# Optimization experiments

Measured on AMD Instinct MI355X. Metric: run time of the kernel, lower is better.

Reference implementation:

```python
import jax, jax.numpy as jnp
import numpy as np

IN_FEATS = 512
OUT_FEATS = 512
N = 8192
M = 8192


def setup_inputs() -> dict:
    key = jax.random.key(0)
    k1, k2, k3 = jax.random.split(key, 3)
    feat_p = jax.random.normal(k1, (N, IN_FEATS), dtype=jnp.float32)
    feat_s = jax.random.normal(k2, (M, IN_FEATS), dtype=jnp.float32)
    # He (kaiming uniform) init: bound = sqrt(6 / fan_in)
    bound = float(np.sqrt(6.0 / IN_FEATS))
    weight_a = jax.random.uniform(k3, (IN_FEATS, OUT_FEATS), dtype=jnp.float32,
                                  minval=-bound, maxval=bound)
    return {"feat_p": feat_p, "feat_s": feat_s, "weight_a": weight_a}


def reference(feat_p, feat_s, weight_a):
    h_i = feat_p @ weight_a            # [N, out]
    h_j = feat_s @ weight_a            # [M, out]
    a_ij = jax.nn.relu(h_i @ h_j.T)    # [N, M]
    fro = jnp.sqrt(jnp.sum(a_ij * a_ij))
    alpha = a_ij / fro                 # global Frobenius-norm normalization
    c_i = alpha @ feat_s               # [N, in]
    return c_i
```

## Files before the change

kernel.cpp:

```cpp
#include <hip/hip_runtime.h>
#include <hip/hip_bf16.h>

#define NROWS 8192
#define DIM   512

typedef short v8s __attribute__((ext_vector_type(8)));
typedef float v4f __attribute__((ext_vector_type(4)));

#define ASM_VMCNT(n) asm volatile("s_waitcnt vmcnt(" #n ")" ::: "memory")
#define ASM_LGKM0    asm volatile("s_waitcnt lgkmcnt(0)" ::: "memory")
#define ASM_FENCE    asm volatile("" ::: "memory")
#define BAR          __builtin_amdgcn_s_barrier()

__device__ __forceinline__ short f2bf(float f) {
    union { float f; unsigned u; } v; v.f = f;
    unsigned r = (v.u + 0x7fffu + ((v.u >> 16) & 1u)) >> 16;
    return (short)r;
}

__device__ __forceinline__ void stage16(const void* g, void* l) {
    typedef __attribute__((address_space(1))) const unsigned GA;
    typedef __attribute__((address_space(3))) unsigned LA;
    __builtin_amdgcn_global_load_lds((GA*)(const unsigned*)g, (LA*)(unsigned*)l, 16, 0, 0);
}

__global__ __launch_bounds__(256) void transpose_cast_kernel(
        const float* __restrict__ in, short* __restrict__ out, int R, int C) {
    __shared__ float t[64][33];
    const int r0 = blockIdx.x * 64;
    const int c0 = blockIdx.y * 32;
    const int lrow = threadIdx.x >> 5;
    const int lcol = threadIdx.x & 31;
#pragma unroll
    for (int p = 0; p < 8; ++p)
        t[lrow + 8 * p][lcol] = in[(size_t)(r0 + lrow + 8 * p) * C + c0 + lcol];
    __syncthreads();
    const int oc = threadIdx.x >> 3;
    const int rb = threadIdx.x & 7;
    v8s o;
#pragma unroll
    for (int e = 0; e < 8; ++e) o[e] = f2bf(t[rb * 8 + e][oc]);
    *(v8s*)(out + (size_t)(c0 + oc) * R + r0 + rb * 8) = o;
}

__global__ __launch_bounds__(256) void gemm1_kernel(
        const float* __restrict__ Fp, const float* __restrict__ Fs,
        const short* __restrict__ WT,
        short* __restrict__ Hp, short* __restrict__ Hs) {
    const float* F = blockIdx.y ? Fs : Fp;
    short* H = blockIdx.y ? Hs : Hp;
    const int lane = threadIdx.x & 63;
    const int wid  = threadIdx.x >> 6;
    const int lr = lane & 15, lg = lane >> 4;
    const int r0 = blockIdx.x * 64 + wid * 16;

    v8s a[16];
#pragma unroll
    for (int kk = 0; kk < 16; ++kk) {
        const float* ap = F + (size_t)(r0 + lr) * DIM + kk * 32 + lg * 8;
        float4 f0 = *(const float4*)ap;
        float4 f1 = *(const float4*)(ap + 4);
        v8s t;
        t[0] = f2bf(f0.x); t[1] = f2bf(f0.y); t[2] = f2bf(f0.z); t[3] = f2bf(f0.w);
        t[4] = f2bf(f1.x); t[5] = f2bf(f1.y); t[6] = f2bf(f1.z); t[7] = f2bf(f1.w);
        a[kk] = t;
    }

    for (int ctp = 0; ctp < 16; ++ctp) {
        const int cb = ctp * 32;
        v4f acc0 = {}, acc1 = {};
#pragma unroll
        for (int kk = 0; kk < 16; ++kk) {
            v8s b0 = *(const v8s*)(WT + (size_t)(cb + lr) * DIM + kk * 32 + lg * 8);
            v8s b1 = *(const v8s*)(WT + (size_t)(cb + 16 + lr) * DIM + kk * 32 + lg * 8);
            acc0 = __builtin_amdgcn_mfma_f32_16x16x32_bf16(a[kk], b0, acc0, 0, 0, 0);
            acc1 = __builtin_amdgcn_mfma_f32_16x16x32_bf16(a[kk], b1, acc1, 0, 0, 0);
        }
#pragma unroll
        for (int i = 0; i < 4; ++i) {
            H[(size_t)(r0 + lg * 4 + i) * DIM + cb + lr]      = f2bf(acc0[i]);
            H[(size_t)(r0 + lg * 4 + i) * DIM + cb + 16 + lr] = f2bf(acc1[i]);
        }
    }
}

#define JSPLIT 2
#define JT_PER_BLOCK (NROWS / 64 / JSPLIT)

__device__ __forceinline__ void stage_full(const char* __restrict__ HsB,
        char* ringW, int j0, int tid) {
#pragma unroll
    for (int s = 0; s < 8; ++s) {
        const int L = s * 8192 + tid * 16;
        const int row = L >> 10;
        const int c = (L & 1023) ^ ((row & 7) << 4);
        stage16(HsB + ((size_t)(j0 + row) << 10) + c, ringW + L);
    }
}

__device__ __forceinline__ void load_bF(v8s (&bF)[8], const short* __restrict__ FsT,
        int j, int wid, int lr, int lg) {
#pragma unroll
    for (int ct = 0; ct < 4; ++ct)
#pragma unroll
        for (int kc2 = 0; kc2 < 2; ++kc2)
            bF[ct * 2 + kc2] = *(const v8s*)(FsT +
                (size_t)(wid * 64 + ct * 16 + lr) * NROWS + j + kc2 * 32 + lg * 8);
}

__device__ __forceinline__ void phase_b(const short (*SbR)[72], const v8s* bF,
        v4f (&accC)[16], int lr, int lg) {
    __builtin_amdgcn_s_setprio(1);
#pragma unroll
    for (int kc2 = 0; kc2 < 2; ++kc2)
#pragma unroll
        for (int mt = 0; mt < 4; ++mt) {
            v8s aS = *(const v8s*)&SbR[mt * 16 + lr][kc2 * 32 + lg * 8];
#pragma unroll
            for (int ct = 0; ct < 4; ++ct)
                accC[mt * 4 + ct] = __builtin_amdgcn_mfma_f32_16x16x32_bf16(
                    aS, bF[ct * 2 + kc2], accC[mt * 4 + ct], 0, 0, 0);
        }
    __builtin_amdgcn_s_setprio(0);
}

__global__ __launch_bounds__(512, 2) void fused_kernel(
        const short* __restrict__ Hp, const short* __restrict__ Hs,
        const short* __restrict__ FsT, float* __restrict__ Cacc,
        float* __restrict__ ssq) {
    __shared__ __align__(16) short HsL[2][64][512];
    __shared__ __align__(16) short Sb[2][64][72];

    const int tid  = threadIdx.x;
    const int lane = tid & 63;
    const int wid  = tid >> 6;
    const int lr = lane & 15, lg = lane >> 4;
    const int strip = wid >> 1;
    const int half  = wid & 1;

    const int nwg = gridDim.x * gridDim.y;
    const int bid = blockIdx.x + gridDim.x * blockIdx.y;
    const int cpx = nwg >> 3;
    const int swz = (bid & 7) * cpx + (bid >> 3);
    const int bx = swz % gridDim.x;
    const int by = swz / gridDim.x;

    const int m0  = bx * 64;
    const int jt0 = by * JT_PER_BLOCK;

    v8s afrag[16];
#pragma unroll
    for (int kk = 0; kk < 16; ++kk)
        afrag[kk] = *(const v8s*)(Hp +
            (size_t)(m0 + strip * 16 + lr) * DIM + kk * 32 + lg * 8);

    v4f accC[16] = {};
    v8s bF[8];
    float ssq_l = 0.f;

    stage_full((const char*)Hs, (char*)&HsL[0][0][0], jt0 * 64, tid);
    ASM_VMCNT(0);

    const int xo = (lr & 7) << 4;

    for (int t = 0; t < JT_PER_BLOCK; ++t) {
        const int jcur  = (jt0 + t) * 64;
        const int jnext = (t + 1 < JT_PER_BLOCK) ? jcur + 64 : jt0 * 64;
        const char* ringR = (const char*)&HsL[t & 1][0][0];
        char*       ringW = (char*)&HsL[(t + 1) & 1][0][0];

        BAR;
        ASM_FENCE;

        stage_full((const char*)Hs, ringW, jnext, tid);

        v4f s0 = {}, s1 = {};
        {
            const char* rp0 = ringR + (size_t)(half * 32 + lr) * 1024;
            const char* rp1 = rp0 + 16 * 1024;
            __builtin_amdgcn_s_setprio(1);
#pragma unroll
            for (int kk = 0; kk < 16; ++kk) {
                const int off = (kk * 64 + lg * 16) ^ xo;
                v8s hb0 = *(const v8s*)(rp0 + off);
                v8s hb1 = *(const v8s*)(rp1 + off);
                s0 = __builtin_amdgcn_mfma_f32_16x16x32_bf16(afrag[kk], hb0, s0, 0, 0, 0);
                s1 = __builtin_amdgcn_mfma_f32_16x16x32_bf16(afrag[kk], hb1, s1, 0, 0, 0);
            }
            __builtin_amdgcn_s_setprio(0);
        }

        short (*SbW)[72] = Sb[t & 1];
#pragma unroll
        for (int i = 0; i < 4; ++i) {
            float v0 = fmaxf(s0[i], 0.f), v1 = fmaxf(s1[i], 0.f);
            ssq_l += v0 * v0 + v1 * v1;
            const int r = strip * 16 + lg * 4 + i;
            SbW[r][(half * 2 + 0) * 16 + lr] = f2bf(v0);
            SbW[r][(half * 2 + 1) * 16 + lr] = f2bf(v1);
        }

        if (t > 0) {
            ASM_VMCNT(8);
            phase_b(Sb[(t - 1) & 1], bF, accC, lr, lg);
        }
        ASM_LGKM0;

        ASM_FENCE;
        load_bF(bF, FsT, jcur, wid, lr, lg);
        ASM_VMCNT(8);
    }

    BAR;
    ASM_VMCNT(0);
    phase_b(Sb[(JT_PER_BLOCK - 1) & 1], bF, accC, lr, lg);

    float w = ssq_l;
#pragma unroll
    for (int off = 32; off; off >>= 1) w += __shfl_down(w, off);
    if (lane == 0) atomicAdd(ssq, w);

#pragma unroll
    for (int mt = 0; mt < 4; ++mt)
#pragma unroll
        for (int ct = 0; ct < 4; ++ct)
#pragma unroll
            for (int i = 0; i < 4; ++i)
                atomicAdd(&Cacc[(size_t)(m0 + mt * 16 + lg * 4 + i) * DIM +
                                wid * 64 + ct * 16 + lr],
                          accC[mt * 4 + ct][i]);
}

__global__ __launch_bounds__(256) void scale_kernel(float* __restrict__ C,
                                                    const float* __restrict__ ssq) {
    const float rs = 1.0f / sqrtf(*ssq);
    const size_t i = (size_t)blockIdx.x * blockDim.x + threadIdx.x;
    float4* p = (float4*)C;
    float4 v = p[i];
    v.x *= rs; v.y *= rs; v.z *= rs; v.w *= rs;
    p[i] = v;
}

extern "C" void kernel_launch(void* const* d_in, const int* in_sizes, int n_in,
                              void* d_out, int out_size, void* d_ws, size_t ws_size,
                              hipStream_t stream) {
    const float* feat_p   = (const float*)d_in[0];
    const float* feat_s   = (const float*)d_in[1];
    const float* weight_a = (const float*)d_in[2];

    char* ws = (char*)d_ws;
    float* ssqp = (float*)ws;
    short* WT   = (short*)(ws + 512);
    short* Hp   = (short*)(ws + 512 + 524288);
    short* Hs   = (short*)(ws + 512 + 524288 + 8388608);
    short* FsT  = (short*)(ws + 512 + 524288 + 16777216);

    transpose_cast_kernel<<<dim3(DIM / 64, DIM / 32), 256, 0, stream>>>(weight_a, WT, DIM, DIM);
    transpose_cast_kernel<<<dim3(NROWS / 64, DIM / 32), 256, 0, stream>>>(feat_s, FsT, NROWS, DIM);

    gemm1_kernel<<<dim3(NROWS / 64, 2), 256, 0, stream>>>(
        feat_p, feat_s, WT, Hp, Hs);

    hipMemsetAsync(d_out, 0, (size_t)out_size * sizeof(float), stream);
    hipMemsetAsync(ssqp, 0, sizeof(float), stream);

    fused_kernel<<<dim3(NROWS / 64, JSPLIT), 512, 0, stream>>>(Hp, Hs, FsT, (float*)d_out, ssqp);

    scale_kernel<<<(out_size / 4 + 255) / 256, 256, 0, stream>>>((float*)d_out, ssqp);
}
```

Measured before the change: 359.7 us.

## Shrink fused kernel tile to 32x32 with 256-thread blocks and split-K accumulators

Reduces the fused GEMM tile from 64 M-rows by 64 J-columns per step to 32x32, using 4 waves per block instead of 8, which doubles the grid size. The phase-A score computation now splits the K loop into even and odd accumulators and sums them, keeping two independent MFMA chains per wave. Phase B is reorganized so each wave covers 128 output columns with 8 B-fragments. The goal is better load balance and occupancy, at the cost of re-reading Hs and FsT twice as often across blocks, more barriers per unit of work, and twice as many atomic adds.

```diff
diff --git a/kernel.cpp b/kernel.cpp
--- a/kernel.cpp
+++ b/kernel.cpp
@@ -84,14 +84,16 @@
     }
 }
 
+#define MTILE  32
+#define JSTEP  32
 #define JSPLIT 2
-#define JT_PER_BLOCK (NROWS / 64 / JSPLIT)
+#define JT_PER_BLOCK (NROWS / JSTEP / JSPLIT)
 
 __device__ __forceinline__ void stage_full(const char* __restrict__ HsB,
         char* ringW, int j0, int tid) {
 #pragma unroll
     for (int s = 0; s < 8; ++s) {
-        const int L = s * 8192 + tid * 16;
+        const int L = s * 4096 + tid * 16;
         const int row = L >> 10;
         const int c = (L & 1023) ^ ((row & 7) << 4);
         stage16(HsB + ((size_t)(j0 + row) << 10) + c, ringW + L);
@@ -101,35 +103,31 @@
 __device__ __forceinline__ void load_bF(v8s (&bF)[8], const short* __restrict__ FsT,
         int j, int wid, int lr, int lg) {
 #pragma unroll
-    for (int ct = 0; ct < 4; ++ct)
-#pragma unroll
-        for (int kc2 = 0; kc2 < 2; ++kc2)
-            bF[ct * 2 + kc2] = *(const v8s*)(FsT +
-                (size_t)(wid * 64 + ct * 16 + lr) * NROWS + j + kc2 * 32 + lg * 8);
-}
-
-__device__ __forceinline__ void phase_b(const short (*SbR)[72], const v8s* bF,
+    for (int ct = 0; ct < 8; ++ct)
+        bF[ct] = *(const v8s*)(FsT +
+            (size_t)(wid * 128 + ct * 16 + lr) * NROWS + j + lg * 8);
+}
+
+__device__ __forceinline__ void phase_b(const short (*SbR)[40], const v8s* bF,
         v4f (&accC)[16], int lr, int lg) {
     __builtin_amdgcn_s_setprio(1);
 #pragma unroll
-    for (int kc2 = 0; kc2 < 2; ++kc2)
-#pragma unroll
-        for (int mt = 0; mt < 4; ++mt) {
-            v8s aS = *(const v8s*)&SbR[mt * 16 + lr][kc2 * 32 + lg * 8];
-#pragma unroll
-            for (int ct = 0; ct < 4; ++ct)
-                accC[mt * 4 + ct] = __builtin_amdgcn_mfma_f32_16x16x32_bf16(
-                    aS, bF[ct * 2 + kc2], accC[mt * 4 + ct], 0, 0, 0);
-        }
+    for (int mt = 0; mt < 2; ++mt) {
+        v8s aS = *(const v8s*)&SbR[mt * 16 + lr][lg * 8];
+#pragma unroll
+        for (int ct = 0; ct < 8; ++ct)
+            accC[mt * 8 + ct] = __builtin_amdgcn_mfma_f32_16x16x32_bf16(
+                aS, bF[ct], accC[mt * 8 + ct], 0, 0, 0);
+    }
     __builtin_amdgcn_s_setprio(0);
 }
 
-__global__ __launch_bounds__(512, 2) void fused_kernel(
+__global__ __launch_bounds__(256, 2) void fused_kernel(
         const short* __restrict__ Hp, const short* __restrict__ Hs,
         const short* __restrict__ FsT, float* __restrict__ Cacc,
         float* __restrict__ ssq) {
-    __shared__ __align__(16) short HsL[2][64][512];
-    __shared__ __align__(16) short Sb[2][64][72];
+    __shared__ __align__(16) short HsL[2][32][512];
+    __shared__ __align__(16) short Sb[2][32][40];
 
     const int tid  = threadIdx.x;
     const int lane = tid & 63;
@@ -145,7 +143,7 @@
     const int bx = swz % gridDim.x;
     const int by = swz / gridDim.x;
 
-    const int m0  = bx * 64;
+    const int m0  = bx * MTILE;
     const int jt0 = by * JT_PER_BLOCK;
 
     v8s afrag[16];
@@ -158,14 +156,14 @@
     v8s bF[8];
     float ssq_l = 0.f;
 
-    stage_full((const char*)Hs, (char*)&HsL[0][0][0], jt0 * 64, tid);
+    stage_full((const char*)Hs, (char*)&HsL[0][0][0], jt0 * JSTEP, tid);
     ASM_VMCNT(0);
 
     const int xo = (lr & 7) << 4;
 
     for (int t = 0; t < JT_PER_BLOCK; ++t) {
-        const int jcur  = (jt0 + t) * 64;
-        const int jnext = (t + 1 < JT_PER_BLOCK) ? jcur + 64 : jt0 * 64;
+        const int jcur  = (jt0 + t) * JSTEP;
+        const int jnext = (t + 1 < JT_PER_BLOCK) ? jcur + JSTEP : jt0 * JSTEP;
         const char* ringR = (const char*)&HsL[t & 1][0][0];
         char*       ringW = (char*)&HsL[(t + 1) & 1][0][0];
 
@@ -174,30 +172,27 @@
 
         stage_full((const char*)Hs, ringW, jnext, tid);
 
-        v4f s0 = {}, s1 = {};
+        v4f sE = {}, sO = {};
         {
-            const char* rp0 = ringR + (size_t)(half * 32 + lr) * 1024;
-            const char* rp1 = rp0 + 16 * 1024;
+            const char* rp = ringR + (size_t)(half * 16 + lr) * 1024;
             __builtin_amdgcn_s_setprio(1);
 #pragma unroll
-            for (int kk = 0; kk < 16; ++kk) {
-                const int off = (kk * 64 + lg * 16) ^ xo;
-                v8s hb0 = *(const v8s*)(rp0 + off);
-                v8s hb1 = *(const v8s*)(rp1 + off);
-                s0 = __builtin_amdgcn_mfma_f32_16x16x32_bf16(afrag[kk], hb0, s0, 0, 0, 0);
-                s1 = __builtin_amdgcn_mfma_f32_16x16x32_bf16(afrag[kk], hb1, s1, 0, 0, 0);
+            for (int kp = 0; kp < 8; ++kp) {
+                const int k0 = 2 * kp, k1 = 2 * kp + 1;
+                v8s hbE = *(const v8s*)(rp + ((k0 * 64 + lg * 16) ^ xo));
+                v8s hbO = *(const v8s*)(rp + ((k1 * 64 + lg * 16) ^ xo));
+                sE = __builtin_amdgcn_mfma_f32_16x16x32_bf16(afrag[k0], hbE, sE, 0, 0, 0);
+                sO = __builtin_amdgcn_mfma_f32_16x16x32_bf16(afrag[k1], hbO, sO, 0, 0, 0);
             }
             __builtin_amdgcn_s_setprio(0);
         }
 
-        short (*SbW)[72] = Sb[t & 1];
+        short (*SbW)[40] = Sb[t & 1];
 #pragma unroll
         for (int i = 0; i < 4; ++i) {
-            float v0 = fmaxf(s0[i], 0.f), v1 = fmaxf(s1[i], 0.f);
-            ssq_l += v0 * v0 + v1 * v1;
-            const int r = strip * 16 + lg * 4 + i;
-            SbW[r][(half * 2 + 0) * 16 + lr] = f2bf(v0);
-            SbW[r][(half * 2 + 1) * 16 + lr] = f2bf(v1);
+            float v = fmaxf(sE[i] + sO[i], 0.f);
+            ssq_l += v * v;
+            SbW[strip * 16 + lg * 4 + i][half * 16 + lr] = f2bf(v);
         }
 
         if (t > 0) {
@@ -221,14 +216,14 @@
     if (lane == 0) atomicAdd(ssq, w);
 
 #pragma unroll
-    for (int mt = 0; mt < 4; ++mt)
-#pragma unroll
-        for (int ct = 0; ct < 4; ++ct)
+    for (int mt = 0; mt < 2; ++mt)
+#pragma unroll
+        for (int ct = 0; ct < 8; ++ct)
 #pragma unroll
             for (int i = 0; i < 4; ++i)
                 atomicAdd(&Cacc[(size_t)(m0 + mt * 16 + lg * 4 + i) * DIM +
-                                wid * 64 + ct * 16 + lr],
-                          accC[mt * 4 + ct][i]);
+                                wid * 128 + ct * 16 + lr],
+                          accC[mt * 8 + ct][i]);
 }
 
 __global__ __launch_bounds__(256) void scale_kernel(float* __restrict__ C,
@@ -264,7 +259,8 @@
     hipMemsetAsync(d_out, 0, (size_t)out_size * sizeof(float), stream);
     hipMemsetAsync(ssqp, 0, sizeof(float), stream);
 
-    fused_kernel<<<dim3(NROWS / 64, JSPLIT), 512, 0, stream>>>(Hp, Hs, FsT, (float*)d_out, ssqp);
+    fused_kernel<<<dim3(NROWS / MTILE, JSPLIT), 256, 0, stream>>>(
+        Hp, Hs, FsT, (float*)d_out, ssqp);
 
     scale_kernel<<<(out_size / 4 + 255) / 256, 256, 0, stream>>>((float*)d_out, ssqp);
 }
```

Result: slower. 464.0 us (+29.0%).

## Split fused attention into materialized S GEMM plus separate C GEMM

Applied to the files above, without the earlier changes.

Replaces the fused kernel (which computed relu(Hp·Hs^T) and multiplied it by feat_s on the fly) with two plain tiled GEMMs when the workspace is large enough. The first writes relu(S) as a 128 MB bf16 matrix and accumulates the sum of squares; the second multiplies S by FsT into the output, so the separate output memset and atomic accumulation go away. The aim is better MFMA tile efficiency and occupancy than the fused kernel, paid for with a large extra round trip of S through HBM. The fused path stays as a fallback when the workspace is too small.

```diff
diff --git a/kernel.cpp b/kernel.cpp
--- a/kernel.cpp
+++ b/kernel.cpp
@@ -84,6 +84,186 @@
     }
 }
 
+__device__ __forceinline__ void stage_t64(const char* __restrict__ src,
+        size_t stride, char* dst, size_t kbyte, int tid) {
+#pragma unroll
+    for (int s = 0; s < 4; ++s) {
+        const int L = s * 4096 + tid * 16;
+        const int row = L >> 7;
+        const int c = (L & 127) ^ ((row & 7) << 4);
+        stage16(src + (size_t)row * stride + kbyte + c, dst + L);
+    }
+}
+
+__device__ __forceinline__ void stage_t128(const char* __restrict__ src,
+        size_t stride, char* dst, size_t kbyte, int tid) {
+#pragma unroll
+    for (int s = 0; s < 8; ++s) {
+        const int L = s * 4096 + tid * 16;
+        const int row = L >> 8;
+        const int c = (L & 255) ^ ((row & 15) << 4);
+        stage16(src + (size_t)row * stride + kbyte + c, dst + L);
+    }
+}
+
+__global__ __launch_bounds__(256, 2) void gemm_s_kernel(
+        const short* __restrict__ Hp, const short* __restrict__ Hs,
+        short* __restrict__ S, float* __restrict__ ssq) {
+    __shared__ __align__(16) short Ab[2][128][64];
+    __shared__ __align__(16) short Bb[2][128][64];
+
+    const int tid = threadIdx.x;
+    const int lane = tid & 63, wq = tid >> 6;
+    const int lr = lane & 15, lg = lane >> 4;
+    const int wm = wq >> 1, wn = wq & 1;
+
+    const int nwg = gridDim.x * gridDim.y;
+    const int bid = blockIdx.x + gridDim.x * blockIdx.y;
+    const int cpx = nwg >> 3;
+    const int swz = (bid & 7) * cpx + (bid >> 3);
+    const int bx = swz % gridDim.x;
+    const int by = swz / gridDim.x;
+    const size_t m0 = (size_t)bx * 128, j0 = (size_t)by * 128;
+
+    const char* Ag = (const char*)Hp + m0 * 1024;
+    const char* Bg = (const char*)Hs + j0 * 1024;
+
+    v4f acc[16] = {};
+
+    stage_t64(Ag, 1024, (char*)&Ab[0][0][0], 0, tid);
+    stage_t64(Bg, 1024, (char*)&Bb[0][0][0], 0, tid);
+    ASM_VMCNT(0);
+
+    const int xo = (lr & 7) << 4;
+    for (int kt = 0; kt < 8; ++kt) {
+        BAR; ASM_FENCE;
+        const size_t kn = (kt + 1 < 8) ? (size_t)(kt + 1) * 128 : 0;
+        stage_t64(Ag, 1024, (char*)&Ab[(kt + 1) & 1][0][0], kn, tid);
+        stage_t64(Bg, 1024, (char*)&Bb[(kt + 1) & 1][0][0], kn, tid);
+
+        const char* Abase = (const char*)&Ab[kt & 1][0][0];
+        const char* Bbase = (const char*)&Bb[kt & 1][0][0];
+        __builtin_amdgcn_s_setprio(1);
+#pragma unroll
+        for (int kc = 0; kc < 2; ++kc) {
+            const int off = (kc * 64 + lg * 16) ^ xo;
+            v8s af[4], bfr[4];
+#pragma unroll
+            for (int mt = 0; mt < 4; ++mt)
+                af[mt] = *(const v8s*)(Abase + (wm * 64 + mt * 16 + lr) * 128 + off);
+#pragma unroll
+            for (int ct = 0; ct < 4; ++ct)
+                bfr[ct] = *(const v8s*)(Bbase + (wn * 64 + ct * 16 + lr) * 128 + off);
+#pragma unroll
+            for (int mt = 0; mt < 4; ++mt)
+#pragma unroll
+                for (int ct = 0; ct < 4; ++ct)
+                    acc[mt * 4 + ct] = __builtin_amdgcn_mfma_f32_16x16x32_bf16(
+                        af[mt], bfr[ct], acc[mt * 4 + ct], 0, 0, 0);
+        }
+        __builtin_amdgcn_s_setprio(0);
+        ASM_LGKM0;
+        ASM_VMCNT(0);
+    }
+
+    BAR;
+    short (*St)[136] = (short (*)[136])&Ab[0][0][0];
+    float ssq_l = 0.f;
+#pragma unroll
+    for (int mt = 0; mt < 4; ++mt)
+#pragma unroll
+        for (int ct = 0; ct < 4; ++ct)
+#pragma unroll
+            for (int i = 0; i < 4; ++i) {
+                float v = fmaxf(acc[mt * 4 + ct][i], 0.f);
+                ssq_l += v * v;
+                St[wm * 64 + mt * 16 + lg * 4 + i][wn * 64 + ct * 16 + lr] = f2bf(v);
+            }
+    ASM_LGKM0; BAR;
+
+    const int row = tid >> 1, hf = tid & 1;
+#pragma unroll
+    for (int s = 0; s < 8; ++s) {
+        v8s d = *(const v8s*)&St[row][hf * 64 + s * 8];
+        *(v8s*)((char*)S + (m0 + row) * (NROWS * 2) + j0 * 2 + hf * 128 + s * 16) = d;
+    }
+
+    float w = ssq_l;
+#pragma unroll
+    for (int off = 32; off; off >>= 1) w += __shfl_down(w, off);
+    if (lane == 0) atomicAdd(ssq, w);
+}
+
+__global__ __launch_bounds__(256, 1) void gemm_c_kernel(
+        const short* __restrict__ S, const short* __restrict__ FsT,
+        float* __restrict__ C) {
+    __shared__ __align__(16) short Ab[2][128][128];
+    __shared__ __align__(16) short Bb[2][128][128];
+
+    const int tid = threadIdx.x;
+    const int lane = tid & 63, wq = tid >> 6;
+    const int lr = lane & 15, lg = lane >> 4;
+    const int wm = wq >> 1, wn = wq & 1;
+
+    const int nwg = gridDim.x * gridDim.y;
+    const int bid = blockIdx.x + gridDim.x * blockIdx.y;
+    const int cpx = nwg >> 3;
+    const int swz = (bid & 7) * cpx + (bid >> 3);
+    const int bx = swz % gridDim.x;
+    const int by = swz / gridDim.x;
+    const size_t m0 = (size_t)bx * 128, n0 = (size_t)by * 128;
+
+    const char* Ag = (const char*)S   + m0 * (NROWS * 2);
+    const char* Bg = (const char*)FsT + n0 * (NROWS * 2);
+
+    v4f acc[16] = {};
+
+    stage_t128(Ag, NROWS * 2, (char*)&Ab[0][0][0], 0, tid);
+    stage_t128(Bg, NROWS * 2, (char*)&Bb[0][0][0], 0, tid);
+    ASM_VMCNT(0);
+
+    const int xo = lr << 4;
+    for (int kt = 0; kt < 64; ++kt) {
+        BAR; ASM_FENCE;
+        const size_t kn = (kt + 1 < 64) ? (size_t)(kt + 1) * 256 : 0;
+        stage_t128(Ag, NROWS * 2, (char*)&Ab[(kt + 1) & 1][0][0], kn, tid);
+        stage_t128(Bg, NROWS * 2, (char*)&Bb[(kt + 1) & 1][0][0], kn, tid);
+
+        const char* Abase = (const char*)&Ab[kt & 1][0][0];
+        const char* Bbase = (const char*)&Bb[kt & 1][0][0];
+        __builtin_amdgcn_s_setprio(1);
+#pragma unroll
+        for (int kc = 0; kc < 4; ++kc) {
+            const int off = (kc * 64 + lg * 16) ^ xo;
+            v8s af[4], bfr[4];
+#pragma unroll
+            for (int mt = 0; mt < 4; ++mt)
+                af[mt] = *(const v8s*)(Abase + (wm * 64 + mt * 16 + lr) * 256 + off);
+#pragma unroll
+            for (int ct = 0; ct < 4; ++ct)
+                bfr[ct] = *(const v8s*)(Bbase + (wn * 64 + ct * 16 + lr) * 256 + off);
+#pragma unroll
+            for (int mt = 0; mt < 4; ++mt)
+#pragma unroll
+                for (int ct = 0; ct < 4; ++ct)
+                    acc[mt * 4 + ct] = __builtin_amdgcn_mfma_f32_16x16x32_bf16(
+                        af[mt], bfr[ct], acc[mt * 4 + ct], 0, 0, 0);
+        }
+        __builtin_amdgcn_s_setprio(0);
+        ASM_LGKM0;
+        ASM_VMCNT(0);
+    }
+
+#pragma unroll
+    for (int mt = 0; mt < 4; ++mt)
+#pragma unroll
+        for (int ct = 0; ct < 4; ++ct)
+#pragma unroll
+            for (int i = 0; i < 4; ++i)
+                C[(m0 + wm * 64 + mt * 16 + lg * 4 + i) * DIM +
+                  n0 + wn * 64 + ct * 16 + lr] = acc[mt * 4 + ct][i];
+}
+
 #define JSPLIT 2
 #define JT_PER_BLOCK (NROWS / 64 / JSPLIT)
 
@@ -171,7 +351,6 @@
 
         BAR;
         ASM_FENCE;
-
         stage_full((const char*)Hs, ringW, jnext, tid);
 
         v4f s0 = {}, s1 = {};
@@ -254,6 +433,9 @@
     short* Hp   = (short*)(ws + 512 + 524288);
     short* Hs   = (short*)(ws + 512 + 524288 + 8388608);
     short* FsT  = (short*)(ws + 512 + 524288 + 16777216);
+    const size_t S_OFF = 512 + 524288 + 3ull * 8388608;
+    short* Smat = (short*)(ws + S_OFF);
+    const size_t need = S_OFF + (size_t)NROWS * NROWS * 2;
 
     transpose_cast_kernel<<<dim3(DIM / 64, DIM / 32), 256, 0, stream>>>(weight_a, WT, DIM, DIM);
     transpose_cast_kernel<<<dim3(NROWS / 64, DIM / 32), 256, 0, stream>>>(feat_s, FsT, NROWS, DIM);
@@ -261,10 +443,18 @@
     gemm1_kernel<<<dim3(NROWS / 64, 2), 256, 0, stream>>>(
         feat_p, feat_s, WT, Hp, Hs);
 
-    hipMemsetAsync(d_out, 0, (size_t)out_size * sizeof(float), stream);
     hipMemsetAsync(ssqp, 0, sizeof(float), stream);
 
-    fused_kernel<<<dim3(NROWS / 64, JSPLIT), 512, 0, stream>>>(Hp, Hs, FsT, (float*)d_out, ssqp);
+    if (ws_size >= need) {
+        gemm_s_kernel<<<dim3(NROWS / 128, NROWS / 128), 256, 0, stream>>>(
+            Hp, Hs, Smat, ssqp);
+        gemm_c_kernel<<<dim3(NROWS / 128, DIM / 128), 256, 0, stream>>>(
+            Smat, FsT, (float*)d_out);
+    } else {
+        hipMemsetAsync(d_out, 0, (size_t)out_size * sizeof(float), stream);
+        fused_kernel<<<dim3(NROWS / 64, JSPLIT), 512, 0, stream>>>(
+            Hp, Hs, FsT, (float*)d_out, ssqp);
+    }
 
     scale_kernel<<<(out_size / 4 + 255) / 256, 256, 0, stream>>>((float*)d_out, ssqp);
 }
```

After: 477.6 us. 1.33x slower.
